# Kernel tuning notes

Measured on AMD Instinct MI355X. Metric: run time of the kernel, lower is better.

The kernel has to match this reference:

```python
import jax, jax.numpy as jnp
import numpy as np
import math

B, S, D, H, L, DFF, VS, VT = 4, 4096, 512, 8, 6, 2048, 69, 69
DK = D // H
NF = max(1, math.ceil(math.log(D)))  # 7
FEAT = 34
EPS = 1e-6


def gelu_approx(x):
    c = math.sqrt(2.0 / math.pi)
    return 0.5 * x * (1.0 + jnp.tanh(c * (x + 0.044715 * x ** 3)))


def layernorm(x, alpha, bias):
    # torch .std() is unbiased (n-1)
    mean = x.mean(axis=-1, keepdims=True)
    var = ((x - mean) ** 2).sum(axis=-1, keepdims=True) / (x.shape[-1] - 1)
    return alpha * (x - mean) / (jnp.sqrt(var) + EPS) + bias


def performer(x, Wq, Wk, Wv, Wo, omega):
    # Wq/Wk/Wv/Wo: [D, D] (torch Linear weight layout, y = x @ W.T)
    q = (x @ Wq.T).reshape(B, S, H, DK)
    k = (x @ Wk.T).reshape(B, S, H, DK)
    v = (x @ Wv.T).reshape(B, S, H, DK)
    qp = jnp.exp(-0.5 * jnp.einsum('bshd,fd->bshf', q, omega) ** 2)
    kp = jnp.exp(-0.5 * jnp.einsum('bshd,fd->bshf', k, omega) ** 2)
    qp = qp / (qp.sum(axis=-1, keepdims=True) + EPS)
    kp = kp / (kp.sum(axis=-1, keepdims=True) + EPS)
    K_cum = jnp.cumsum(kp, axis=1)                                   # [B,S,H,F]
    KV_cum = jnp.cumsum(kp[..., None] * v[..., None, :], axis=1)     # [B,S,H,F,DK]
    # block_size_h = block_size_w = 1 -> key_indices = arange(S) clamped
    key_idx = jnp.clip(jnp.arange(S), 0, S - 1)
    K_sel = K_cum[:, key_idx]
    KV_sel = KV_cum[:, key_idx]
    num = jnp.einsum('bshf,bshfd->bshd', qp, KV_sel)
    den = jnp.einsum('bshf,bshf->bsh', qp, K_sel)[..., None]
    out = (num / (den + EPS)).reshape(B, S, D)
    return out @ Wo.T


def pos_encoding():
    pos = jnp.arange(S, dtype=jnp.float32)[:, None]
    div = jnp.exp(jnp.arange(0, D, 2, dtype=jnp.float32) * (-math.log(10000.0) / D))
    pe = jnp.zeros((S, D), dtype=jnp.float32)
    pe = pe.at[:, 0::2].set(jnp.sin(pos * div))
    pe = pe.at[:, 1::2].set(jnp.cos(pos * div))
    return pe


def setup_inputs():
    key = jax.random.key(0)
    ks = jax.random.split(key, 16)
    sc = 0.02
    token_ids = jax.random.randint(ks[0], (B, S), 0, VS)
    id_embed = jax.random.normal(ks[1], (VS, D), jnp.float32) * sc
    feat_proj_w = jax.random.normal(ks[2], (D, FEAT), jnp.float32) * sc
    feature_table = jnp.zeros((VS, FEAT), jnp.float32)  # module's global feature_array is zeros
    product_mask = jnp.zeros((VS,), bool).at[jnp.arange(13, 57)].set(True)
    wq = jax.random.normal(ks[3], (L, D, D), jnp.float32) * sc
    wk = jax.random.normal(ks[4], (L, D, D), jnp.float32) * sc
    wv = jax.random.normal(ks[5], (L, D, D), jnp.float32) * sc
    wo = jax.random.normal(ks[6], (L, D, D), jnp.float32) * sc
    omega = jax.random.normal(ks[7], (L, NF, DK), jnp.float32) / math.sqrt(DK)
    ln1_a = jnp.ones((L, D)); ln1_b = jnp.zeros((L, D))
    ln2_a = jnp.ones((L, D)); ln2_b = jnp.zeros((L, D))
    w1 = jax.random.normal(ks[8], (L, DFF, D), jnp.float32) * sc
    b1 = jnp.zeros((L, DFF))
    w2 = jax.random.normal(ks[9], (L, D, DFF), jnp.float32) * sc
    b2 = jnp.zeros((L, D))
    fin_a = jnp.ones((D,)); fin_b = jnp.zeros((D,))
    proj_w = jax.random.normal(ks[10], (VT, D), jnp.float32) * sc
    proj_b = jnp.zeros((VT,))
    return dict(token_ids=token_ids, id_embed=id_embed, feat_proj_w=feat_proj_w,
                feature_table=feature_table, product_mask=product_mask,
                wq=wq, wk=wk, wv=wv, wo=wo, omega=omega,
                ln1_a=ln1_a, ln1_b=ln1_b, ln2_a=ln2_a, ln2_b=ln2_b,
                w1=w1, b1=b1, w2=w2, b2=b2, fin_a=fin_a, fin_b=fin_b,
                proj_w=proj_w, proj_b=proj_b)


def reference(token_ids, id_embed, feat_proj_w, feature_table, product_mask,
              wq, wk, wv, wo, omega, ln1_a, ln1_b, ln2_a, ln2_b,
              w1, b1, w2, b2, fin_a, fin_b, proj_w, proj_b):
    # SpecialPlusFeatureLookup: id embedding + (masked) projected product features
    id_vec = id_embed[token_ids]                                  # [B,S,D]
    feats = feature_table[token_ids] @ feat_proj_w.T              # [B,S,D]
    feat_vec = jnp.where(product_mask[token_ids][..., None], feats, 0.0)
    x = id_vec + feat_vec + pos_encoding()[None]
    for i in range(L):
        xn = layernorm(x, ln1_a[i], ln1_b[i])
        x = x + performer(xn, wq[i], wk[i], wv[i], wo[i], omega[i])
        xn2 = layernorm(x, ln2_a[i], ln2_b[i])
        ff = gelu_approx(xn2 @ w1[i].T + b1[i]) @ w2[i].T + b2[i]
        x = x + ff
    x = layernorm(x, fin_a, fin_b)
    return x @ proj_w.T + proj_b                                  # [B,S,VT]
```

## Files before the change

### kernel.cpp

```cpp
#include <hip/hip_runtime.h>
#include <hip/hip_bf16.h>
#include <math.h>

#define Bsz   4
#define Ssz   4096
#define Dsz   512
#define Hsz   8
#define Lsz   6
#define DFFsz 2048
#define VTsz  69
#define VSsz  69
#define DKsz  64
#define NFsz  7
#define FEATsz 34
#define EPSf  1e-6f
#define CSsz  32
#define NCsz  128
#define Msz   (Bsz*Ssz)
#define QKVN  1536

typedef __hip_bfloat16 bf16;
using bf16x8 = __attribute__((ext_vector_type(8))) __bf16;
using f32x4  = __attribute__((ext_vector_type(4))) float;

#define GLOAD16(gp, lp)                                                        \
  __builtin_amdgcn_global_load_lds(                                            \
      (const __attribute__((address_space(1))) unsigned int*)(gp),             \
      (__attribute__((address_space(3))) unsigned int*)(lp), 16, 0, 0)

__device__ __forceinline__ unsigned short f2bf_bits(float f) {
  unsigned int u = __float_as_uint(f);
  u += 0x7fffu + ((u >> 16) & 1u);
  return (unsigned short)(u >> 16);
}
__device__ __forceinline__ float gelu_f(float x) {
  const float c2 = 1.5957691216057308f;
  float u = c2 * (x + 0.044715f * x * x * x);
  return x / (1.0f + __expf(-u));
}

__global__ void detect_kernel(const unsigned int* __restrict__ p, int* __restrict__ flag) {
  if (threadIdx.x == 0 && blockIdx.x == 0) *flag = (p[0] == 0x3F800000u) ? 0 : 1;
}
__device__ __forceinline__ float load_as_f32(const void* p, int i, int flag) {
  if (flag == 0) return ((const float*)p)[i];
  unsigned int u = ((const unsigned short*)p)[i];
  return __uint_as_float(u << 16);
}

#define OFF_OM    0
#define OFF_L1A   2688
#define OFF_L1B   5760
#define OFF_L2A   8832
#define OFF_L2B   11904
#define OFF_B1    14976
#define OFF_B2    27264
#define OFF_FINA  30336
#define OFF_FINB  30848
#define OFF_IDE   31360
#define OFF_FPW   66688
#define OFF_FTAB  84096
#define SMALL_TOT 86442
__global__ __launch_bounds__(256) void cvt_smalls_kernel(
    const void* om, const void* l1a, const void* l1b, const void* l2a,
    const void* l2b, const void* b1, const void* b2, const void* fina,
    const void* finb, const void* idE, const void* fpw, const void* ftab,
    float* __restrict__ dst, const int* __restrict__ flag) {
  int i = blockIdx.x * 256 + threadIdx.x;
  if (i >= SMALL_TOT) return;
  const void* src; int off;
  if      (i < OFF_L1A)  { src = om;   off = OFF_OM; }
  else if (i < OFF_L1B)  { src = l1a;  off = OFF_L1A; }
  else if (i < OFF_L2A)  { src = l1b;  off = OFF_L1B; }
  else if (i < OFF_L2B)  { src = l2a;  off = OFF_L2A; }
  else if (i < OFF_B1)   { src = l2b;  off = OFF_L2B; }
  else if (i < OFF_B2)   { src = b1;   off = OFF_B1; }
  else if (i < OFF_FINA) { src = b2;   off = OFF_B2; }
  else if (i < OFF_FINB) { src = fina; off = OFF_FINA; }
  else if (i < OFF_IDE)  { src = finb; off = OFF_FINB; }
  else if (i < OFF_FPW)  { src = idE;  off = OFF_IDE; }
  else if (i < OFF_FTAB) { src = fpw;  off = OFF_FPW; }
  else                   { src = ftab; off = OFF_FTAB; }
  dst[i] = load_as_f32(src, i - off, *flag);
}

#define WO_N  (Lsz*Dsz*Dsz)
#define W1_N  (Lsz*DFFsz*Dsz)
#define W2_N  (Lsz*Dsz*DFFsz)
#define W3_TOT (WO_N + W1_N + W2_N)
__global__ __launch_bounds__(256) void cvt_w3_kernel(const void* wo,
    const void* w1, const void* w2, unsigned short* __restrict__ dst,
    const int* __restrict__ flag) {
  int i = blockIdx.x * 256 + threadIdx.x;
  if (i >= W3_TOT) return;
  const void* src; int off;
  if      (i < WO_N)        { src = wo; off = 0; }
  else if (i < WO_N + W1_N) { src = w1; off = WO_N; }
  else                      { src = w2; off = WO_N + W1_N; }
  if (*flag == 0) dst[i] = f2bf_bits(((const float*)src)[i - off]);
  else            dst[i] = ((const unsigned short*)src)[i - off];
}

__global__ __launch_bounds__(256) void pack_qkv_kernel(const void* __restrict__ wq,
    const void* __restrict__ wk, const void* __restrict__ wv,
    unsigned short* __restrict__ dst, const int* __restrict__ flag) {
  int gid = blockIdx.x * 256 + threadIdx.x;
  int l = gid / (QKVN * Dsz);
  int rem = gid - l * (QKVN * Dsz);
  int r = rem >> 9;
  int d = rem & 511;
  const void* src = (r < 512) ? wq : (r < 1024) ? wk : wv;
  int rr = (r < 512) ? r : (r < 1024) ? r - 512 : r - 1024;
  float v = load_as_f32(src, l * (Dsz * Dsz) + rr * Dsz + d, *flag);
  dst[gid] = f2bf_bits(v);
}
__global__ __launch_bounds__(256) void pad_pw_kernel(const void* __restrict__ pw,
    const void* __restrict__ pb, unsigned short* __restrict__ pwp,
    float* __restrict__ pbp, const int* __restrict__ flag) {
  int gid = blockIdx.x * 256 + threadIdx.x;
  int n = gid >> 9, d = gid & 511;
  float v = (n < VTsz) ? load_as_f32(pw, n * Dsz + d, *flag) : 0.0f;
  pwp[gid] = f2bf_bits(v);
  if (gid < 128) pbp[gid] = (gid < VTsz) ? load_as_f32(pb, gid, *flag) : 0.0f;
}

__global__ __launch_bounds__(256) void tokvec_kernel(const float* __restrict__ idE,
    const float* __restrict__ fpw, const float* __restrict__ ftab,
    float* __restrict__ tokvec) {
  int gid = blockIdx.x * 256 + threadIdx.x;
  int tk = gid >> 9, d = gid & 511;
  float fs = 0.0f;
  #pragma unroll
  for (int j = 0; j < FEATsz; ++j)
    fs += ftab[tk * FEATsz + j] * fpw[d * FEATsz + j];
  tokvec[gid] = idE[gid] + fs;
}
__global__ __launch_bounds__(256) void embed_kernel(const int* __restrict__ tok,
    const float* __restrict__ tokvec, float* __restrict__ x) {
  int gid = blockIdx.x * 256 + threadIdx.x;
  int p = gid & 255, bs = gid >> 8;
  int tk = tok[bs];
  float div = __expf(-0.035977892078f * (float)p);
  float sv, cv;
  __sincosf((float)(bs & (Ssz - 1)) * div, &sv, &cv);
  float2 tv = ((const float2*)tokvec)[tk * 256 + p];
  float2 o; o.x = tv.x + sv; o.y = tv.y + cv;
  ((float2*)x)[gid] = o;
}

__global__ __launch_bounds__(256) void ln_kernel(const float* __restrict__ x,
    const float* __restrict__ ga, const float* __restrict__ gb, bf16* __restrict__ out) {
  __shared__ float red[8];
  const int row = blockIdx.x;
  const int t = threadIdx.x;
  float2 v = ((const float2*)(x + (size_t)row * Dsz))[t];
  float s = v.x + v.y;
  #pragma unroll
  for (int o = 32; o > 0; o >>= 1) s += __shfl_down(s, o, 64);
  if ((t & 63) == 0) red[t >> 6] = s;
  __syncthreads();
  if (t == 0) red[4] = (red[0] + red[1] + red[2] + red[3]) * (1.0f / Dsz);
  __syncthreads();
  const float mean = red[4];
  float d0 = v.x - mean, d1 = v.y - mean;
  float q = d0 * d0 + d1 * d1;
  #pragma unroll
  for (int o = 32; o > 0; o >>= 1) q += __shfl_down(q, o, 64);
  __syncthreads();
  if ((t & 63) == 0) red[t >> 6] = q;
  __syncthreads();
  if (t == 0) red[4] = red[0] + red[1] + red[2] + red[3];
  __syncthreads();
  const float inv = 1.0f / (sqrtf(red[4] * (1.0f / (Dsz - 1))) + EPSf);
  float2 gav = ((const float2*)ga)[t];
  float2 gbv = ((const float2*)gb)[t];
  ushort2 o2;
  o2.x = f2bf_bits(gav.x * (d0 * inv) + gbv.x);
  o2.y = f2bf_bits(gav.y * (d1 * inv) + gbv.y);
  ((ushort2*)out)[(size_t)row * 256 + t] = o2;
}

template<int KT, bool BIAS, bool GELUACT, int OUT>
__global__ __launch_bounds__(256) void gemm_bt(
    const bf16* __restrict__ A, const bf16* __restrict__ Bw,
    const float* __restrict__ bias, bf16* __restrict__ Obf,
    float* __restrict__ Of, int N) {
  __shared__ __attribute__((aligned(128))) char lds[32768];
  const int t = threadIdx.x;
  const int lane = t & 63;
  const int wm = t >> 7;
  const int wn = (t >> 6) & 1;
  const int gx = gridDim.x;
  const int nwg = gx * gridDim.y;
  int f = blockIdx.y * gx + blockIdx.x;
  f = ((f & 7) * (nwg >> 3)) + (f >> 3);
  const int tileN = (f % gx) * 128;
  const int tileM = (f / gx) * 128;

  f32x4 acc[4][4];
  f32x4 zz = {0.f, 0.f, 0.f, 0.f};
  #pragma unroll
  for (int i = 0; i < 4; ++i)
    #pragma unroll
    for (int j = 0; j < 4; ++j) acc[i][j] = zz;

  const int r_st = t >> 3;
  const int kgs  = (t & 7) ^ (r_st & 7);
  const bf16* gA0 = A  + (size_t)(tileM + r_st) * KT + kgs * 8;
  const bf16* gB0 = Bw + (size_t)(tileN + r_st) * KT + kgs * 8;
  const int rowA = (wm * 64 + (lane & 15)) << 7;
  const int rowB = 16384 + ((wn * 64 + (lane & 15)) << 7);
  const int xo0 = (((lane >> 4) ^ (lane & 7)) << 4);
  const int xo1 = (((4 + (lane >> 4)) ^ (lane & 7)) << 4);

  #pragma unroll
  for (int kt = 0; kt < KT; kt += 64) {
    __syncthreads();
    #pragma unroll
    for (int it = 0; it < 4; ++it) {
      GLOAD16(gA0 + (size_t)(it * 32) * KT + kt, lds +         it * 4096 + t * 16);
      GLOAD16(gB0 + (size_t)(it * 32) * KT + kt, lds + 16384 + it * 4096 + t * 16);
    }
    __syncthreads();
    #pragma unroll
    for (int ks = 0; ks < 2; ++ks) {
      const int xo = ks ? xo1 : xo0;
      bf16x8 af[4], bfv[4];
      #pragma unroll
      for (int mi = 0; mi < 4; ++mi)
        af[mi] = *(const bf16x8*)(lds + rowA + mi * 2048 + xo);
      #pragma unroll
      for (int ni = 0; ni < 4; ++ni)
        bfv[ni] = *(const bf16x8*)(lds + rowB + ni * 2048 + xo);
      #pragma unroll
      for (int mi = 0; mi < 4; ++mi)
        #pragma unroll
        for (int ni = 0; ni < 4; ++ni)
          acc[mi][ni] = __builtin_amdgcn_mfma_f32_16x16x32_bf16(
              af[mi], bfv[ni], acc[mi][ni], 0, 0, 0);
    }
  }

  if (OUT == 0) {
    __syncthreads();
    #pragma unroll
    for (int mi = 0; mi < 4; ++mi)
      #pragma unroll
      for (int ni = 0; ni < 4; ++ni) {
        const int col = wn * 64 + ni * 16 + (lane & 15);
        const float bv = BIAS ? bias[tileN + col] : 0.0f;
        #pragma unroll
        for (int j = 0; j < 4; ++j) {
          const int row = wm * 64 + mi * 16 + ((lane >> 4) << 2) + j;
          float vv = acc[mi][ni][j] + bv;
          if (GELUACT) vv = gelu_f(vv);
          *(unsigned short*)(lds + (size_t)row * 256 +
                             ((col * 2) ^ (((row >> 2) & 7) << 5))) = f2bf_bits(vv);
        }
      }
    __syncthreads();
    #pragma unroll
    for (int p = 0; p < 8; ++p) {
      const int flat = p * 4096 + t * 16;
      const int row = flat >> 8, cb = flat & 255;
      uint4 v = *(const uint4*)(lds + (size_t)row * 256 + (cb ^ (((row >> 2) & 7) << 5)));
      *(uint4*)((char*)(Obf + (size_t)(tileM + row) * N + tileN) + cb) = v;
    }
  } else {
    const int rBase = tileM + wm * 64 + ((lane >> 4) << 2);
    const int cBase = tileN + wn * 64 + (lane & 15);
    #pragma unroll
    for (int ni = 0; ni < 4; ++ni) {
      const int col = cBase + ni * 16;
      const float bv = BIAS ? bias[col] : 0.0f;
      #pragma unroll
      for (int mi = 0; mi < 4; ++mi) {
        #pragma unroll
        for (int j = 0; j < 4; ++j) {
          const int rr2 = rBase + mi * 16 + j;
          float vv = acc[mi][ni][j] + bv;
          if (GELUACT) vv = gelu_f(vv);
          if (OUT == 1) Of[(size_t)rr2 * N + col] += vv;
          else          Of[(size_t)rr2 * N + col] = vv;
        }
      }
    }
  }
}

__device__ __forceinline__ void featrow_to_lds(const bf16* __restrict__ rowp,
    const float* __restrict__ om, float* __restrict__ dst, int lane) {
  const int srow = lane >> 1, half = lane & 1;
  const bf16x8* r8 = (const bf16x8*)rowp;
  float v[32];
  #pragma unroll
  for (int j = 0; j < 4; ++j) {
    bf16x8 a = r8[j];
    #pragma unroll
    for (int u = 0; u < 8; ++u) v[j * 8 + u] = (float)a[u];
  }
  float tt[NFsz]; float ssum = 0.f;
  #pragma unroll
  for (int ff = 0; ff < NFsz; ++ff) {
    const float* orow = om + ff * DKsz + half * 32;
    float d = 0.f;
    #pragma unroll
    for (int u = 0; u < 32; ++u) d += v[u] * orow[u];
    d += __shfl_xor(d, 1, 64);
    float e = __expf(-0.5f * d * d);
    tt[ff] = e; ssum += e;
  }
  float inv = 1.0f / (ssum + EPSf);
  if (half == 0) {
    #pragma unroll
    for (int ff = 0; ff < NFsz; ++ff) dst[srow * NFsz + ff] = tt[ff] * inv;
  }
}

__global__ __launch_bounds__(256) void pscan_partial(
    const bf16* __restrict__ qkv, const float* __restrict__ om,
    float* __restrict__ kvS, float* __restrict__ kS) {
  __shared__ float skp[4][CSsz * NFsz];
  const int w = threadIdx.x >> 6;
  const int lane = threadIdx.x & 63;
  const int cid = blockIdx.x * 4 + w;
  const int c = cid & (NCsz - 1);
  const int bh = cid >> 7;
  const int h = bh & (Hsz - 1);
  const int b = bh >> 3;
  const int s0 = c * CSsz;
  featrow_to_lds(qkv + (size_t)(b * Ssz + s0 + (lane >> 1)) * QKVN + 512
                     + h * DKsz + (lane & 1) * 32,
                 om, skp[w], lane);
  asm volatile("s_waitcnt lgkmcnt(0)" ::: "memory");
  float st[NFsz], ks[NFsz];
  #pragma unroll
  for (int ff = 0; ff < NFsz; ++ff) { st[ff] = 0.f; ks[ff] = 0.f; }
  const bf16* vb = qkv + (size_t)(b * Ssz + s0) * QKVN + 1024 + h * DKsz + lane;
  for (int s = 0; s < CSsz; ++s) {
    const float vv = __bfloat162float(vb[(size_t)s * QKVN]);
    #pragma unroll
    for (int ff = 0; ff < NFsz; ++ff) {
      float kf = skp[w][s * NFsz + ff];
      st[ff] += kf * vv;
      ks[ff] += kf;
    }
  }
  float* kvo = kvS + (size_t)cid * (NFsz * DKsz);
  #pragma unroll
  for (int ff = 0; ff < NFsz; ++ff) kvo[ff * DKsz + lane] = st[ff];
  if (lane < NFsz) {
    float val = 0.f;
    #pragma unroll
    for (int ff = 0; ff < NFsz; ++ff) val = (lane == ff) ? ks[ff] : val;
    kS[(size_t)cid * NFsz + lane] = val;
  }
}

__global__ __launch_bounds__(512) void pscan_scan(float* __restrict__ kvS, float* __restrict__ kS) {
  const int bh = blockIdx.x;
  const int comp = threadIdx.x;
  if (comp < NFsz * DKsz) {
    float run = 0.f;
    size_t base = (size_t)bh * NCsz * (NFsz * DKsz) + comp;
    #pragma unroll 8
    for (int c = 0; c < NCsz; ++c) {
      size_t ix = base + (size_t)c * (NFsz * DKsz);
      float tv = kvS[ix]; kvS[ix] = run; run += tv;
    }
  } else if (comp < NFsz * DKsz + NFsz) {
    int ff = comp - NFsz * DKsz;
    float run = 0.f;
    #pragma unroll 8
    for (int c = 0; c < NCsz; ++c) {
      size_t ix = (size_t)bh * NCsz * NFsz + ff + (size_t)c * NFsz;
      float tv = kS[ix]; kS[ix] = run; run += tv;
    }
  }
}

__global__ __launch_bounds__(256) void pscan_out(
    const bf16* __restrict__ qkv, const float* __restrict__ om,
    const float* __restrict__ kvS, const float* __restrict__ kS,
    bf16* __restrict__ attn) {
  __shared__ float skp[4][CSsz * NFsz];
  __shared__ float sqp[4][CSsz * NFsz];
  const int w = threadIdx.x >> 6;
  const int lane = threadIdx.x & 63;
  const int cid = blockIdx.x * 4 + w;
  const int c = cid & (NCsz - 1);
  const int bh = cid >> 7;
  const int h = bh & (Hsz - 1);
  const int b = bh >> 3;
  const int s0 = c * CSsz;
  const bf16* rowbase = qkv + (size_t)(b * Ssz + s0 + (lane >> 1)) * QKVN
                            + h * DKsz + (lane & 1) * 32;
  featrow_to_lds(rowbase,       om, sqp[w], lane);
  featrow_to_lds(rowbase + 512, om, skp[w], lane);
  asm volatile("s_waitcnt lgkmcnt(0)" ::: "memory");
  float kvst[NFsz], kst[NFsz];
  #pragma unroll
  for (int ff = 0; ff < NFsz; ++ff) kvst[ff] = kvS[(size_t)cid * (NFsz * DKsz) + ff * DKsz + lane];
  #pragma unroll
  for (int ff = 0; ff < NFsz; ++ff) kst[ff] = kS[(size_t)cid * NFsz + ff];
  const bf16* vb = qkv + (size_t)(b * Ssz + s0) * QKVN + 1024 + h * DKsz + lane;
  bf16* ob = attn + (size_t)(b * Ssz + s0) * Dsz + h * DKsz + lane;
  for (int s = 0; s < CSsz; ++s) {
    const float vv = __bfloat162float(vb[(size_t)s * QKVN]);
    float num = 0.f, den = 0.f;
    #pragma unroll
    for (int ff = 0; ff < NFsz; ++ff) {
      float kf = skp[w][s * NFsz + ff];
      kvst[ff] += kf * vv;
      kst[ff]  += kf;
      float qf = sqp[w][s * NFsz + ff];
      num += qf * kvst[ff];
      den += qf * kst[ff];
    }
    ob[(size_t)s * Dsz] = __float2bfloat16(num / (den + EPSf));
  }
}

__global__ __launch_bounds__(256) void proj_finish(const float* __restrict__ pt,
    void* __restrict__ out, const int* __restrict__ flag) {
  int gid = blockIdx.x * 256 + threadIdx.x;
  if (gid >= Msz * VTsz) return;
  int m = gid / VTsz, n = gid - m * VTsz;
  float r = pt[(size_t)m * 128 + n];
  if (*flag == 0) ((float*)out)[gid] = r;
  else            ((unsigned short*)out)[gid] = f2bf_bits(r);
}

extern "C" void kernel_launch(void* const* d_in, const int* in_sizes, int n_in,
                              void* d_out, int out_size, void* d_ws, size_t ws_size,
                              hipStream_t stream) {
  (void)in_sizes; (void)n_in; (void)out_size; (void)ws_size;
  const int* tok = (const int*)d_in[0];

  char* ws = (char*)d_ws;
  size_t off = 0;
  auto take = [&](size_t bytes) -> char* {
    char* p = ws + off; off += (bytes + 255) & ~(size_t)255; return p;
  };
  float* x    = (float*)take((size_t)Msz * Dsz * 4);
  bf16*  xn   = (bf16*) take((size_t)Msz * Dsz * 2);
  bf16*  hbuf = (bf16*) take((size_t)Msz * DFFsz * 2);
  bf16*  qkv  = (bf16*) take((size_t)Msz * QKVN * 2);
  float* kvS  = (float*)take((size_t)Bsz * Hsz * NCsz * NFsz * DKsz * 4);
  float* kS   = (float*)take((size_t)Bsz * Hsz * NCsz * NFsz * 4);
  float* ptmp = (float*)take((size_t)Msz * 128 * 4);
  bf16*  wqkvb= (bf16*) take((size_t)Lsz * QKVN * Dsz * 2);
  bf16*  w3   = (bf16*) take((size_t)W3_TOT * 2);
  bf16*  pwp  = (bf16*) take((size_t)128 * Dsz * 2);
  float* pbp  = (float*)take((size_t)128 * 4);
  float* tokv = (float*)take((size_t)VSsz * Dsz * 4);
  float* smalls = (float*)take((size_t)SMALL_TOT * 4);
  int*   flag = (int*)  take(16);

  bf16* wob = w3;
  bf16* w1b = w3 + WO_N;
  bf16* w2b = w3 + WO_N + W1_N;
  float* omF  = smalls + OFF_OM;
  float* l1aF = smalls + OFF_L1A;
  float* l1bF = smalls + OFF_L1B;
  float* l2aF = smalls + OFF_L2A;
  float* l2bF = smalls + OFF_L2B;
  float* b1F  = smalls + OFF_B1;
  float* b2F  = smalls + OFF_B2;
  float* finaF= smalls + OFF_FINA;
  float* finbF= smalls + OFF_FINB;
  float* idEF = smalls + OFF_IDE;
  float* fpwF = smalls + OFF_FPW;
  float* ftabF= smalls + OFF_FTAB;

  detect_kernel<<<1, 1, 0, stream>>>((const unsigned int*)d_in[10], flag);
  pack_qkv_kernel<<<(Lsz * QKVN * Dsz) / 256, 256, 0, stream>>>(
      d_in[5], d_in[6], d_in[7], (unsigned short*)wqkvb, flag);
  cvt_w3_kernel<<<(W3_TOT + 255) / 256, 256, 0, stream>>>(
      d_in[8], d_in[14], d_in[16], (unsigned short*)w3, flag);
  cvt_smalls_kernel<<<(SMALL_TOT + 255) / 256, 256, 0, stream>>>(
      d_in[9], d_in[10], d_in[11], d_in[12], d_in[13], d_in[15], d_in[17],
      d_in[18], d_in[19], d_in[1], d_in[2], d_in[3], smalls, flag);
  pad_pw_kernel<<<(128 * Dsz) / 256, 256, 0, stream>>>(d_in[20], d_in[21],
      (unsigned short*)pwp, pbp, flag);

  tokvec_kernel<<<(VSsz * Dsz) / 256, 256, 0, stream>>>(idEF, fpwF, ftabF, tokv);
  embed_kernel<<<Msz, 256, 0, stream>>>(tok, tokv, x);

  dim3 gQKV(QKVN / 128, Msz / 128);
  dim3 gO  (Dsz  / 128, Msz / 128);
  dim3 gFF1(DFFsz/ 128, Msz / 128);
  dim3 gFF2(Dsz  / 128, Msz / 128);
  dim3 gPRJ(1, Msz / 128);
  for (int i = 0; i < Lsz; ++i) {
    ln_kernel<<<Msz, 256, 0, stream>>>(x, l1aF + i * Dsz, l1bF + i * Dsz, xn);
    gemm_bt<512, false, false, 0><<<gQKV, 256, 0, stream>>>(
        xn, wqkvb + (size_t)i * QKVN * Dsz, nullptr, qkv, nullptr, QKVN);
    pscan_partial<<<Bsz * Hsz * NCsz / 4, 256, 0, stream>>>(
        qkv, omF + (size_t)i * NFsz * DKsz, kvS, kS);
    pscan_scan<<<Bsz * Hsz, 512, 0, stream>>>(kvS, kS);
    pscan_out<<<Bsz * Hsz * NCsz / 4, 256, 0, stream>>>(
        qkv, omF + (size_t)i * NFsz * DKsz, kvS, kS, hbuf);
    gemm_bt<512, false, false, 1><<<gO, 256, 0, stream>>>(
        hbuf, wob + (size_t)i * Dsz * Dsz, nullptr, nullptr, x, Dsz);
    ln_kernel<<<Msz, 256, 0, stream>>>(x, l2aF + i * Dsz, l2bF + i * Dsz, xn);
    gemm_bt<512, true, true, 0><<<gFF1, 256, 0, stream>>>(
        xn, w1b + (size_t)i * DFFsz * Dsz, b1F + i * DFFsz, hbuf, nullptr, DFFsz);
    gemm_bt<2048, true, false, 1><<<gFF2, 256, 0, stream>>>(
        hbuf, w2b + (size_t)i * Dsz * DFFsz, b2F + i * Dsz, nullptr, x, Dsz);
  }
  ln_kernel<<<Msz, 256, 0, stream>>>(x, finaF, finbF, xn);
  gemm_bt<512, true, false, 2><<<gPRJ, 256, 0, stream>>>(
      xn, pwp, pbp, nullptr, ptmp, 128);
  proj_finish<<<(Msz * VTsz + 255) / 256, 256, 0, stream>>>(ptmp, d_out, flag);
}
```

Before: 1.692 ms.

## Use wave-per-row layernorm, split scan across blocks, fuse projection output conversion

LayerNorm now handles one row per wavefront with float4 loads and xor-shuffle reductions, which removes the LDS round trips and block barriers. The chunk scan is spread over 256 small blocks instead of 32 large ones, giving more parallelism for the serial per-component loop. The final projection GEMM writes the 69-column output directly in the requested dtype, which removes the temporary buffer and the separate proj_finish kernel. Each of these cuts launch overhead or synchronisation in small memory-bound kernels.

```diff
diff --git a/kernel.cpp b/kernel.cpp
--- a/kernel.cpp
+++ b/kernel.cpp
@@ -150,41 +150,42 @@
 
 __global__ __launch_bounds__(256) void ln_kernel(const float* __restrict__ x,
     const float* __restrict__ ga, const float* __restrict__ gb, bf16* __restrict__ out) {
-  __shared__ float red[8];
-  const int row = blockIdx.x;
-  const int t = threadIdx.x;
-  float2 v = ((const float2*)(x + (size_t)row * Dsz))[t];
-  float s = v.x + v.y;
-  #pragma unroll
-  for (int o = 32; o > 0; o >>= 1) s += __shfl_down(s, o, 64);
-  if ((t & 63) == 0) red[t >> 6] = s;
-  __syncthreads();
-  if (t == 0) red[4] = (red[0] + red[1] + red[2] + red[3]) * (1.0f / Dsz);
-  __syncthreads();
-  const float mean = red[4];
-  float d0 = v.x - mean, d1 = v.y - mean;
-  float q = d0 * d0 + d1 * d1;
-  #pragma unroll
-  for (int o = 32; o > 0; o >>= 1) q += __shfl_down(q, o, 64);
-  __syncthreads();
-  if ((t & 63) == 0) red[t >> 6] = q;
-  __syncthreads();
-  if (t == 0) red[4] = red[0] + red[1] + red[2] + red[3];
-  __syncthreads();
-  const float inv = 1.0f / (sqrtf(red[4] * (1.0f / (Dsz - 1))) + EPSf);
-  float2 gav = ((const float2*)ga)[t];
-  float2 gbv = ((const float2*)gb)[t];
-  ushort2 o2;
-  o2.x = f2bf_bits(gav.x * (d0 * inv) + gbv.x);
-  o2.y = f2bf_bits(gav.y * (d1 * inv) + gbv.y);
-  ((ushort2*)out)[(size_t)row * 256 + t] = o2;
+  const int w = threadIdx.x >> 6, lane = threadIdx.x & 63;
+  const size_t row = (size_t)blockIdx.x * 4 + w;
+  const float4* xr = (const float4*)(x + row * Dsz);
+  float4 a = xr[lane], b = xr[lane + 64];
+  float s = a.x + a.y + a.z + a.w + b.x + b.y + b.z + b.w;
+  #pragma unroll
+  for (int o = 32; o > 0; o >>= 1) s += __shfl_xor(s, o, 64);
+  const float mean = s * (1.0f / Dsz);
+  float dx0 = a.x - mean, dx1 = a.y - mean, dx2 = a.z - mean, dx3 = a.w - mean;
+  float dy0 = b.x - mean, dy1 = b.y - mean, dy2 = b.z - mean, dy3 = b.w - mean;
+  float q = dx0*dx0 + dx1*dx1 + dx2*dx2 + dx3*dx3
+          + dy0*dy0 + dy1*dy1 + dy2*dy2 + dy3*dy3;
+  #pragma unroll
+  for (int o = 32; o > 0; o >>= 1) q += __shfl_xor(q, o, 64);
+  const float inv = 1.0f / (sqrtf(q * (1.0f / (Dsz - 1))) + EPSf);
+  float4 g0 = ((const float4*)ga)[lane], g1 = ((const float4*)ga)[lane + 64];
+  float4 h0 = ((const float4*)gb)[lane], h1 = ((const float4*)gb)[lane + 64];
+  ushort4 o0, o1;
+  o0.x = f2bf_bits(g0.x * (dx0 * inv) + h0.x);
+  o0.y = f2bf_bits(g0.y * (dx1 * inv) + h0.y);
+  o0.z = f2bf_bits(g0.z * (dx2 * inv) + h0.z);
+  o0.w = f2bf_bits(g0.w * (dx3 * inv) + h0.w);
+  o1.x = f2bf_bits(g1.x * (dy0 * inv) + h1.x);
+  o1.y = f2bf_bits(g1.y * (dy1 * inv) + h1.y);
+  o1.z = f2bf_bits(g1.z * (dy2 * inv) + h1.z);
+  o1.w = f2bf_bits(g1.w * (dy3 * inv) + h1.w);
+  ((ushort4*)(out + row * Dsz))[lane]      = o0;
+  ((ushort4*)(out + row * Dsz))[lane + 64] = o1;
 }
 
 template<int KT, bool BIAS, bool GELUACT, int OUT>
 __global__ __launch_bounds__(256) void gemm_bt(
     const bf16* __restrict__ A, const bf16* __restrict__ Bw,
     const float* __restrict__ bias, bf16* __restrict__ Obf,
-    float* __restrict__ Of, int N) {
+    float* __restrict__ Of, int N,
+    const int* __restrict__ flag = nullptr, void* __restrict__ vout = nullptr) {
   __shared__ __attribute__((aligned(128))) char lds[32768];
   const int t = threadIdx.x;
   const int lane = t & 63;
@@ -265,6 +266,26 @@
       const int row = flat >> 8, cb = flat & 255;
       uint4 v = *(const uint4*)(lds + (size_t)row * 256 + (cb ^ (((row >> 2) & 7) << 5)));
       *(uint4*)((char*)(Obf + (size_t)(tileM + row) * N + tileN) + cb) = v;
+    }
+  } else if (OUT == 3) {
+    const int fl = *flag;
+    const int rBase = tileM + wm * 64 + ((lane >> 4) << 2);
+    const int cBase = tileN + wn * 64 + (lane & 15);
+    #pragma unroll
+    for (int ni = 0; ni < 4; ++ni) {
+      const int col = cBase + ni * 16;
+      const float bv = BIAS ? bias[col] : 0.0f;
+      if (col < VTsz) {
+        #pragma unroll
+        for (int mi = 0; mi < 4; ++mi)
+          #pragma unroll
+          for (int j = 0; j < 4; ++j) {
+            const int row = rBase + mi * 16 + j;
+            float vv = acc[mi][ni][j] + bv;
+            if (fl == 0) ((float*)vout)[(size_t)row * VTsz + col] = vv;
+            else ((unsigned short*)vout)[(size_t)row * VTsz + col] = f2bf_bits(vv);
+          }
+      }
     }
   } else {
     const int rBase = tileM + wm * 64 + ((lane >> 4) << 2);
@@ -357,9 +378,9 @@
   }
 }
 
-__global__ __launch_bounds__(512) void pscan_scan(float* __restrict__ kvS, float* __restrict__ kS) {
-  const int bh = blockIdx.x;
-  const int comp = threadIdx.x;
+__global__ __launch_bounds__(64) void pscan_scan(float* __restrict__ kvS, float* __restrict__ kS) {
+  const int bh = blockIdx.x >> 3;
+  const int comp = ((blockIdx.x & 7) << 6) + threadIdx.x;
   if (comp < NFsz * DKsz) {
     float run = 0.f;
     size_t base = (size_t)bh * NCsz * (NFsz * DKsz) + comp;
@@ -421,16 +442,6 @@
   }
 }
 
-__global__ __launch_bounds__(256) void proj_finish(const float* __restrict__ pt,
-    void* __restrict__ out, const int* __restrict__ flag) {
-  int gid = blockIdx.x * 256 + threadIdx.x;
-  if (gid >= Msz * VTsz) return;
-  int m = gid / VTsz, n = gid - m * VTsz;
-  float r = pt[(size_t)m * 128 + n];
-  if (*flag == 0) ((float*)out)[gid] = r;
-  else            ((unsigned short*)out)[gid] = f2bf_bits(r);
-}
-
 extern "C" void kernel_launch(void* const* d_in, const int* in_sizes, int n_in,
                               void* d_out, int out_size, void* d_ws, size_t ws_size,
                               hipStream_t stream) {
@@ -448,7 +459,6 @@
   bf16*  qkv  = (bf16*) take((size_t)Msz * QKVN * 2);
   float* kvS  = (float*)take((size_t)Bsz * Hsz * NCsz * NFsz * DKsz * 4);
   float* kS   = (float*)take((size_t)Bsz * Hsz * NCsz * NFsz * 4);
-  float* ptmp = (float*)take((size_t)Msz * 128 * 4);
   bf16*  wqkvb= (bf16*) take((size_t)Lsz * QKVN * Dsz * 2);
   bf16*  w3   = (bf16*) take((size_t)W3_TOT * 2);
   bf16*  pwp  = (bf16*) take((size_t)128 * Dsz * 2);
@@ -493,24 +503,23 @@
   dim3 gFF2(Dsz  / 128, Msz / 128);
   dim3 gPRJ(1, Msz / 128);
   for (int i = 0; i < Lsz; ++i) {
-    ln_kernel<<<Msz, 256, 0, stream>>>(x, l1aF + i * Dsz, l1bF + i * Dsz, xn);
+    ln_kernel<<<Msz / 4, 256, 0, stream>>>(x, l1aF + i * Dsz, l1bF + i * Dsz, xn);
     gemm_bt<512, false, false, 0><<<gQKV, 256, 0, stream>>>(
         xn, wqkvb + (size_t)i * QKVN * Dsz, nullptr, qkv, nullptr, QKVN);
     pscan_partial<<<Bsz * Hsz * NCsz / 4, 256, 0, stream>>>(
         qkv, omF + (size_t)i * NFsz * DKsz, kvS, kS);
-    pscan_scan<<<Bsz * Hsz, 512, 0, stream>>>(kvS, kS);
+    pscan_scan<<<Bsz * Hsz * 8, 64, 0, stream>>>(kvS, kS);
     pscan_out<<<Bsz * Hsz * NCsz / 4, 256, 0, stream>>>(
         qkv, omF + (size_t)i * NFsz * DKsz, kvS, kS, hbuf);
     gemm_bt<512, false, false, 1><<<gO, 256, 0, stream>>>(
         hbuf, wob + (size_t)i * Dsz * Dsz, nullptr, nullptr, x, Dsz);
-    ln_kernel<<<Msz, 256, 0, stream>>>(x, l2aF + i * Dsz, l2bF + i * Dsz, xn);
+    ln_kernel<<<Msz / 4, 256, 0, stream>>>(x, l2aF + i * Dsz, l2bF + i * Dsz, xn);
     gemm_bt<512, true, true, 0><<<gFF1, 256, 0, stream>>>(
         xn, w1b + (size_t)i * DFFsz * Dsz, b1F + i * DFFsz, hbuf, nullptr, DFFsz);
     gemm_bt<2048, true, false, 1><<<gFF2, 256, 0, stream>>>(
         hbuf, w2b + (size_t)i * Dsz * DFFsz, b2F + i * Dsz, nullptr, x, Dsz);
   }
-  ln_kernel<<<Msz, 256, 0, stream>>>(x, finaF, finbF, xn);
-  gemm_bt<512, true, false, 2><<<gPRJ, 256, 0, stream>>>(
-      xn, pwp, pbp, nullptr, ptmp, 128);
-  proj_finish<<<(Msz * VTsz + 255) / 256, 256, 0, stream>>>(ptmp, d_out, flag);
-}
+  ln_kernel<<<Msz / 4, 256, 0, stream>>>(x, finaF, finbF, xn);
+  gemm_bt<512, true, false, 3><<<gPRJ, 256, 0, stream>>>(
+      xn, pwp, pbp, nullptr, nullptr, 128, flag, d_out);
+}
```

After: 1.586 ms. 1.07x faster.
